# Kernel optimization log

Hardware: AMD Instinct MI355X
Metric: run time of the kernel (lower is better)

Reference implementation:

```python
import jax, jax.numpy as jnp
import numpy as np

N_NODES = 50000
N_EDGES = 800000
D = 64
N_GRAPHS = 512
N_LAYERS = 3
HID_FC = 64
N_CLASSES = 10


def setup_inputs() -> dict:
    key = jax.random.key(0)
    ks = jax.random.split(key, 12)
    s = 1.0 / np.sqrt(D)
    x = jax.random.normal(ks[0], (N_NODES, D), dtype=jnp.float32)
    edge_index = jax.random.randint(ks[1], (2, N_EDGES), 0, N_NODES, dtype=jnp.int32)
    batch = jnp.sort(jax.random.randint(ks[2], (N_NODES,), 0, N_GRAPHS, dtype=jnp.int32))
    convW1 = jax.random.normal(ks[3], (N_LAYERS, D, D), dtype=jnp.float32) * s
    convb1 = jax.random.normal(ks[4], (N_LAYERS, D), dtype=jnp.float32) * 0.01
    convW2 = jax.random.normal(ks[5], (N_LAYERS, D, D), dtype=jnp.float32) * s
    convb2 = jax.random.normal(ks[6], (N_LAYERS, D), dtype=jnp.float32) * 0.01
    fcW1 = jax.random.normal(ks[7], (D, HID_FC), dtype=jnp.float32) * s
    fcb1 = jax.random.normal(ks[8], (HID_FC,), dtype=jnp.float32) * 0.01
    fcW2 = jax.random.normal(ks[9], (HID_FC, N_CLASSES), dtype=jnp.float32) * (1.0 / np.sqrt(HID_FC))
    fcb2 = jax.random.normal(ks[10], (N_CLASSES,), dtype=jnp.float32) * 0.01
    return {"x": x, "convW1": convW1, "convb1": convb1, "convW2": convW2,
            "convb2": convb2, "fcW1": fcW1, "fcb1": fcb1, "fcW2": fcW2,
            "fcb2": fcb2, "edge_index": edge_index, "batch": batch}


def reference(x, convW1, convb1, convW2, convb2, fcW1, fcb1, fcW2, fcb2, edge_index, batch):
    src, dst = edge_index[0], edge_index[1]
    h = x
    for l in range(N_LAYERS):
        # GIN aggregation: (1 + eps) * x + sum_{j in N(i)} x_j, eps = 0
        agg = jax.ops.segment_sum(h[src], dst, num_segments=N_NODES)
        h = h + agg
        # per-layer MLP: Linear -> ReLU -> Linear
        h = jax.nn.relu(h @ convW1[l] + convb1[l])
        h = h @ convW2[l] + convb2[l]
    # global max pool over nodes of each graph
    g = jax.ops.segment_max(h, batch, num_segments=N_GRAPHS)
    # FC head: Linear(64) -> ReLU -> Linear(num_classes)
    g = jax.nn.relu(g @ fcW1 + fcb1)
    logits = g @ fcW2 + fcb2
    return jax.nn.log_softmax(logits, axis=1)
```

## Files before the change

### kernel.cpp

```cpp
#include <hip/hip_runtime.h>
#include <math.h>

#define N_NODES 50000
#define N_EDGES 800000
#define D 64
#define N_GRAPHS 512
#define N_CLASSES 10
#define NT 3125

#define SCAN_B 512
#define NB_SCAN ((N_NODES + SCAN_B - 1) / SCAN_B)

typedef __attribute__((ext_vector_type(8))) short bf16x8;
typedef __attribute__((ext_vector_type(4))) float f32x4;

#define MFMA16(a, b, c) __builtin_amdgcn_mfma_f32_16x16x32_bf16(a, b, c, 0, 0, 0)


__device__ __forceinline__ unsigned mapf(float f) {
  unsigned u = __float_as_uint(f);
  return (u & 0x80000000u) ? ~u : (u | 0x80000000u);
}
__device__ __forceinline__ float unmapf(unsigned u) {
  return __uint_as_float((u & 0x80000000u) ? (u & 0x7FFFFFFFu) : ~u);
}
__device__ __forceinline__ ushort bf16_rne(float f) {
  unsigned u = __float_as_uint(f);
  u += 0x7FFFu + ((u >> 16) & 1u);
  return (ushort)(u >> 16);
}
__device__ __forceinline__ float bf16_tof(ushort h) {
  return __uint_as_float(((unsigned)h) << 16);
}
__device__ __forceinline__ unsigned pack2(float a, float b) {
  return (unsigned)bf16_rne(a) | ((unsigned)bf16_rne(b) << 16);
}
__device__ __forceinline__ float2 unpack2(unsigned v) {
  return make_float2(__uint_as_float(v << 16), __uint_as_float(v & 0xFFFF0000u));
}


__global__ void to_bf16(const float* __restrict__ in, unsigned* __restrict__ out) {
  int i = blockIdx.x * 256 + threadIdx.x;
  float4 v = reinterpret_cast<const float4*>(in)[i];
  reinterpret_cast<uint2*>(out)[i] = make_uint2(pack2(v.x, v.y), pack2(v.z, v.w));
}


__global__ void wprep(const float* __restrict__ convW1, const float* __restrict__ convW2,
                      ushort* __restrict__ wf) {
  const int wi = blockIdx.x;
  const int layer = wi >> 1, which = wi & 1;
  const float* W = (which ? convW2 : convW1) + layer * 4096;
  const int t = threadIdx.x;
  const int f = t >> 6, lane = t & 63;
  const int ct = f >> 1, ks = f & 1;
  const int n = ct * 16 + (lane & 15);
  const int k0 = ks * 32 + ((lane >> 4) << 3);
  ushort hi[8], lo[8];
#pragma unroll
  for (int v = 0; v < 8; ++v) {
    float w = W[(k0 + v) * 64 + n];
    ushort h = bf16_rne(w);
    hi[v] = h;
    lo[v] = bf16_rne(w - bf16_tof(h));
  }
  ushort* base = wf + layer * 16384 + which * 8192;
  *(uint4*)(base + f * 512 + lane * 8) = *(uint4*)hi;
  *(uint4*)(base + 4096 + f * 512 + lane * 8) = *(uint4*)lo;
}


__global__ void hist_kernel(const int* __restrict__ dst, int* __restrict__ deg) {
  int e = blockIdx.x * 256 + threadIdx.x;
  if (e < N_EDGES) atomicAdd(&deg[dst[e]], 1);
}

__global__ void scan_blocks(const int* __restrict__ deg, int* __restrict__ bsum) {
  __shared__ int sd[SCAN_B];
  int i = blockIdx.x * SCAN_B + threadIdx.x;
  sd[threadIdx.x] = (i < N_NODES) ? deg[i] : 0;
  __syncthreads();
  for (int off = SCAN_B / 2; off > 0; off >>= 1) {
    if (threadIdx.x < off) sd[threadIdx.x] += sd[threadIdx.x + off];
    __syncthreads();
  }
  if (threadIdx.x == 0) bsum[blockIdx.x] = sd[0];
}

__global__ void scan_mid(int* __restrict__ bsum) {
  __shared__ int s[256];
  int t = threadIdx.x;
  if (t < NB_SCAN) s[t] = bsum[t];
  __syncthreads();
  if (t == 0) {
    int run = 0;
    for (int i = 0; i < NB_SCAN; ++i) { int v = s[i]; s[i] = run; run += v; }
  }
  __syncthreads();
  if (t < NB_SCAN) bsum[t] = s[t];
}

__global__ void scan_final(const int* __restrict__ deg, const int* __restrict__ bsum,
                           int* __restrict__ rs, int* __restrict__ cur) {
  __shared__ int sd[SCAN_B];
  int i = blockIdx.x * SCAN_B + threadIdx.x;
  int v = (i < N_NODES) ? deg[i] : 0;
  sd[threadIdx.x] = v;
  __syncthreads();
  for (int off = 1; off < SCAN_B; off <<= 1) {
    int add = (threadIdx.x >= off) ? sd[threadIdx.x - off] : 0;
    __syncthreads();
    sd[threadIdx.x] += add;
    __syncthreads();
  }
  if (i < N_NODES) {
    int ex = bsum[blockIdx.x] + sd[threadIdx.x] - v;
    rs[i] = ex;
    cur[i] = ex;
  }
  if (i == 0) rs[N_NODES] = N_EDGES;
}

__global__ void fill_csr(const int* __restrict__ src, const int* __restrict__ dst,
                         int* __restrict__ cur, int* __restrict__ csr) {
  int e = blockIdx.x * 256 + threadIdx.x;
  if (e >= N_EDGES) return;
  int p = atomicAdd(&cur[dst[e]], 1);
  csr[p] = src[e];
}


__global__ __launch_bounds__(256) void agg_bf16(
    const unsigned* __restrict__ hin, const int* __restrict__ csr,
    const int* __restrict__ rs, unsigned* __restrict__ hout) {
  const int t = threadIdx.x;
  const int hw = t >> 5, hl = t & 31;
  const int node = blockIdx.x * 8 + hw;
  float2 a = unpack2(hin[node * 32 + hl]);
  int e = rs[node];
  const int e1 = rs[node + 1];
  for (; e + 4 <= e1; e += 4) {
    int s0 = csr[e], s1 = csr[e + 1], s2 = csr[e + 2], s3 = csr[e + 3];
    float2 v0 = unpack2(hin[s0 * 32 + hl]);
    float2 v1 = unpack2(hin[s1 * 32 + hl]);
    float2 v2 = unpack2(hin[s2 * 32 + hl]);
    float2 v3 = unpack2(hin[s3 * 32 + hl]);
    a.x += v0.x + v1.x; a.y += v0.y + v1.y;
    a.x += v2.x + v3.x; a.y += v2.y + v3.y;
  }
  for (; e < e1; ++e) {
    float2 v = unpack2(hin[csr[e] * 32 + hl]);
    a.x += v.x; a.y += v.y;
  }
  hout[node * 32 + hl] = pack2(a.x, a.y);
}


template <int FINAL>
__global__ __launch_bounds__(256, 4) void mlp_bf16(
    unsigned* __restrict__ A,
    const ushort* __restrict__ wfL,
    const float* __restrict__ b1, const float* __restrict__ b2,
    const int* __restrict__ batch, unsigned* __restrict__ gU) {
  __shared__ ushort Wl[8192];
  __shared__ ushort tb[4][16 * 72];
  const int t = threadIdx.x;
  const int w = t >> 6, lane = t & 63;
  const int tile = blockIdx.x * 4 + w;
  const bool act = (tile < NT);
  const int m = lane & 15, g = lane >> 4;
  ushort* tw = tb[w];

  {
    const uint4* s = (const uint4*)wfL;
    uint4* d = (uint4*)Wl;
#pragma unroll
    for (int i = 0; i < 4; ++i) d[t + 256 * i] = s[t + 256 * i];
  }

  bf16x8 a0 = {}, a1 = {};
  if (act) {
    const ushort* Ar = (const ushort*)A + (size_t)(tile * 16 + m) * 64;
    a0 = *(const bf16x8*)(Ar + g * 8);
    a1 = *(const bf16x8*)(Ar + 32 + g * 8);
  }
  __syncthreads();

  const char* wb = (const char*)Wl + lane * 16;
#define LDW(off) (*(const bf16x8*)(wb + (off)))

  f32x4 c0 = {0.f, 0.f, 0.f, 0.f}, c1 = c0, c2 = c0, c3 = c0;
  bf16x8 h0 = {}, h1 = {};
  if (act) {
#define G1(ct, cc)                                     \
    cc = MFMA16(a0, LDW((2 * ct + 0) * 1024), cc);     \
    cc = MFMA16(a1, LDW((2 * ct + 1) * 1024), cc);     \
    cc = MFMA16(a0, LDW(8192 + (2 * ct + 0) * 1024), cc); \
    cc = MFMA16(a1, LDW(8192 + (2 * ct + 1) * 1024), cc);
    G1(0, c0) G1(1, c1) G1(2, c2) G1(3, c3)
#undef G1

    float bv0 = b1[m], bv1 = b1[16 + m], bv2 = b1[32 + m], bv3 = b1[48 + m];
#define WRT(cc, ct, bv)                                               \
    tw[(g * 4 + 0) * 72 + ct * 16 + m] = bf16_rne(fmaxf(cc[0] + bv, 0.f)); \
    tw[(g * 4 + 1) * 72 + ct * 16 + m] = bf16_rne(fmaxf(cc[1] + bv, 0.f)); \
    tw[(g * 4 + 2) * 72 + ct * 16 + m] = bf16_rne(fmaxf(cc[2] + bv, 0.f)); \
    tw[(g * 4 + 3) * 72 + ct * 16 + m] = bf16_rne(fmaxf(cc[3] + bv, 0.f));
    WRT(c0, 0, bv0) WRT(c1, 1, bv1) WRT(c2, 2, bv2) WRT(c3, 3, bv3)
#undef WRT
    h0 = *(const bf16x8*)(tw + m * 72 + g * 8);
    h1 = *(const bf16x8*)(tw + m * 72 + 32 + g * 8);
  }
  __syncthreads();

  {
    const uint4* s = (const uint4*)(wfL + 8192);
    uint4* d = (uint4*)Wl;
#pragma unroll
    for (int i = 0; i < 4; ++i) d[t + 256 * i] = s[t + 256 * i];
  }
  __syncthreads();

  if (act) {
    c0 = (f32x4){0.f, 0.f, 0.f, 0.f}; c1 = c0; c2 = c0; c3 = c0;
#define G2(ct, cc)                                     \
    cc = MFMA16(h0, LDW((2 * ct + 0) * 1024), cc);     \
    cc = MFMA16(h1, LDW((2 * ct + 1) * 1024), cc);     \
    cc = MFMA16(h0, LDW(8192 + (2 * ct + 0) * 1024), cc); \
    cc = MFMA16(h1, LDW(8192 + (2 * ct + 1) * 1024), cc);
    G2(0, c0) G2(1, c1) G2(2, c2) G2(3, c3)
#undef G2
#undef LDW

    float bv0 = b2[m], bv1 = b2[16 + m], bv2 = b2[32 + m], bv3 = b2[48 + m];
    if (FINAL) {
      int b40 = batch[tile * 16 + g * 4 + 0];
      int b41 = batch[tile * 16 + g * 4 + 1];
      int b42 = batch[tile * 16 + g * 4 + 2];
      int b43 = batch[tile * 16 + g * 4 + 3];
#define PM(cc, ct, bv)                                          \
      atomicMax(&gU[b40 * 64 + ct * 16 + m], mapf(cc[0] + bv)); \
      atomicMax(&gU[b41 * 64 + ct * 16 + m], mapf(cc[1] + bv)); \
      atomicMax(&gU[b42 * 64 + ct * 16 + m], mapf(cc[2] + bv)); \
      atomicMax(&gU[b43 * 64 + ct * 16 + m], mapf(cc[3] + bv));
      PM(c0, 0, bv0) PM(c1, 1, bv1) PM(c2, 2, bv2) PM(c3, 3, bv3)
#undef PM
    } else {
#define WRO(cc, ct, bv)                                    \
      tw[(g * 4 + 0) * 72 + ct * 16 + m] = bf16_rne(cc[0] + bv); \
      tw[(g * 4 + 1) * 72 + ct * 16 + m] = bf16_rne(cc[1] + bv); \
      tw[(g * 4 + 2) * 72 + ct * 16 + m] = bf16_rne(cc[2] + bv); \
      tw[(g * 4 + 3) * 72 + ct * 16 + m] = bf16_rne(cc[3] + bv);
      WRO(c0, 0, bv0) WRO(c1, 1, bv1) WRO(c2, 2, bv2) WRO(c3, 3, bv3)
#undef WRO
      uint4 v0 = *(const uint4*)(tw + m * 72 + g * 16);
      uint4 v1 = *(const uint4*)(tw + m * 72 + g * 16 + 8);
      uint4* Aw = (uint4*)((ushort*)A + (size_t)(tile * 16 + m) * 64 + g * 16);
      Aw[0] = v0;
      Aw[1] = v1;
    }
  }
}


__global__ void init_g(unsigned* __restrict__ gU) {
  int i = blockIdx.x * blockDim.x + threadIdx.x;
  if (i < N_GRAPHS * D) gU[i] = 0x007FFFFFu;
}

__global__ void head_kernel(const unsigned* __restrict__ gU,
                            const float* __restrict__ fcW1, const float* __restrict__ fcb1,
                            const float* __restrict__ fcW2, const float* __restrict__ fcb2,
                            float* __restrict__ out) {
  __shared__ float gbuf[64];
  __shared__ float hid[64];
  __shared__ float logit[N_CLASSES];
  __shared__ float red[2];
  const int gi = blockIdx.x;
  const int t = threadIdx.x;

  gbuf[t] = unmapf(gU[gi * D + t]);
  __syncthreads();

  float a = fcb1[t];
#pragma unroll
  for (int k = 0; k < 64; ++k) a = fmaf(gbuf[k], fcW1[k * 64 + t], a);
  hid[t] = fmaxf(a, 0.0f);
  __syncthreads();

  if (t < N_CLASSES) {
    float l = fcb2[t];
#pragma unroll
    for (int k = 0; k < 64; ++k) l = fmaf(hid[k], fcW2[k * N_CLASSES + t], l);
    logit[t] = l;
  }
  __syncthreads();

  if (t == 0) {
    float mx = logit[0];
    for (int i = 1; i < N_CLASSES; ++i) mx = fmaxf(mx, logit[i]);
    float s = 0.0f;
    for (int i = 0; i < N_CLASSES; ++i) s += expf(logit[i] - mx);
    red[0] = mx;
    red[1] = logf(s);
  }
  __syncthreads();

  if (t < N_CLASSES) out[gi * N_CLASSES + t] = logit[t] - red[0] - red[1];
}


extern "C" void kernel_launch(void* const* d_in, const int* in_sizes, int n_in,
                              void* d_out, int out_size, void* d_ws, size_t ws_size,
                              hipStream_t stream) {
  const float* x      = (const float*)d_in[0];
  const float* convW1 = (const float*)d_in[1];
  const float* convb1 = (const float*)d_in[2];
  const float* convW2 = (const float*)d_in[3];
  const float* convb2 = (const float*)d_in[4];
  const float* fcW1   = (const float*)d_in[5];
  const float* fcb1   = (const float*)d_in[6];
  const float* fcW2   = (const float*)d_in[7];
  const float* fcb2   = (const float*)d_in[8];
  const int*   edge   = (const int*)d_in[9];
  const int*   batch  = (const int*)d_in[10];
  float* out = (float*)d_out;

  const int* src = edge;
  const int* dst = edge + N_EDGES;

  unsigned* xb  = (unsigned*)d_ws;
  unsigned* hbA = xb + (size_t)N_NODES * 32;
  unsigned* gU  = hbA + (size_t)N_NODES * 32;
  int* rs  = (int*)(gU + N_GRAPHS * D);
  int* csr = rs + N_NODES + 1;
  ushort* wf = (ushort*)(csr + N_EDGES);
  int* deg  = (int*)hbA;
  int* cur  = deg + N_NODES;
  int* bsum = cur + N_NODES;

  to_bf16<<<(N_NODES * 16) / 256, 256, 0, stream>>>(x, xb);
  wprep<<<6, 512, 0, stream>>>(convW1, convW2, wf);
  init_g<<<(N_GRAPHS * D + 255) / 256, 256, 0, stream>>>(gU);

  hipMemsetAsync(deg, 0, N_NODES * sizeof(int), stream);
  hist_kernel<<<N_EDGES / 256, 256, 0, stream>>>(dst, deg);
  scan_blocks<<<NB_SCAN, SCAN_B, 0, stream>>>(deg, bsum);
  scan_mid<<<1, 256, 0, stream>>>(bsum);
  scan_final<<<NB_SCAN, SCAN_B, 0, stream>>>(deg, bsum, rs, cur);
  fill_csr<<<N_EDGES / 256, 256, 0, stream>>>(src, dst, cur, csr);

  const int AGG_B = N_NODES / 8;
  const int MLP_B = (NT + 3) / 4;
  agg_bf16<<<AGG_B, 256, 0, stream>>>(xb, csr, rs, hbA);
  mlp_bf16<0><<<MLP_B, 256, 0, stream>>>(hbA, wf, convb1, convb2, batch, gU);
  agg_bf16<<<AGG_B, 256, 0, stream>>>(hbA, csr, rs, xb);
  mlp_bf16<0><<<MLP_B, 256, 0, stream>>>(xb, wf + 16384, convb1 + 64, convb2 + 64,
                                         batch, gU);
  agg_bf16<<<AGG_B, 256, 0, stream>>>(xb, csr, rs, hbA);
  mlp_bf16<1><<<MLP_B, 256, 0, stream>>>(hbA, wf + 32768, convb1 + 128, convb2 + 128,
                                         batch, gU);

  head_kernel<<<N_GRAPHS, 64, 0, stream>>>(gU, fcW1, fcb1, fcW2, fcb2, out);
}
```

Measured before the change: 242.6 us.

## Partition CSR build by destination range and preload both MLP weights once

```diff
diff --git a/kernel.cpp b/kernel.cpp
--- a/kernel.cpp
+++ b/kernel.cpp
@@ -7,6 +7,7 @@
 #define N_GRAPHS 512
 #define N_CLASSES 10
 #define NT 3125
+#define NPART 6250
 
 #define SCAN_B 512
 #define NB_SCAN ((N_NODES + SCAN_B - 1) / SCAN_B)
@@ -71,9 +72,14 @@
 }
 
 
-__global__ void hist_kernel(const int* __restrict__ dst, int* __restrict__ deg) {
-  int e = blockIdx.x * 256 + threadIdx.x;
-  if (e < N_EDGES) atomicAdd(&deg[dst[e]], 1);
+__global__ void hist_part(const int* __restrict__ dst, int* __restrict__ deg) {
+  const int p = blockIdx.x & 7;
+  const int lo = p * NPART, hi = lo + NPART;
+  const int stride = (gridDim.x >> 3) * 256;
+  for (int e = (blockIdx.x >> 3) * 256 + threadIdx.x; e < N_EDGES; e += stride) {
+    int d = dst[e];
+    if (d >= lo && d < hi) atomicAdd(&deg[d], 1);
+  }
 }
 
 __global__ void scan_blocks(const int* __restrict__ deg, int* __restrict__ bsum) {
@@ -122,12 +128,18 @@
   if (i == 0) rs[N_NODES] = N_EDGES;
 }
 
-__global__ void fill_csr(const int* __restrict__ src, const int* __restrict__ dst,
-                         int* __restrict__ cur, int* __restrict__ csr) {
-  int e = blockIdx.x * 256 + threadIdx.x;
-  if (e >= N_EDGES) return;
-  int p = atomicAdd(&cur[dst[e]], 1);
-  csr[p] = src[e];
+__global__ void fill_part(const int* __restrict__ src, const int* __restrict__ dst,
+                          int* __restrict__ cur, int* __restrict__ csr) {
+  const int p = blockIdx.x & 7;
+  const int lo = p * NPART, hi = lo + NPART;
+  const int stride = (gridDim.x >> 3) * 256;
+  for (int e = (blockIdx.x >> 3) * 256 + threadIdx.x; e < N_EDGES; e += stride) {
+    int d = dst[e];
+    if (d >= lo && d < hi) {
+      int pos = atomicAdd(&cur[d], 1);
+      csr[pos] = src[e];
+    }
+  }
 }
 
 
@@ -158,12 +170,13 @@
 
 
 template <int FINAL>
-__global__ __launch_bounds__(256, 4) void mlp_bf16(
-    unsigned* __restrict__ A,
+__global__ __launch_bounds__(256, 2) void mlp_bf16(
+    const unsigned* __restrict__ Ain,
+    unsigned* __restrict__ Aout,
     const ushort* __restrict__ wfL,
     const float* __restrict__ b1, const float* __restrict__ b2,
     const int* __restrict__ batch, unsigned* __restrict__ gU) {
-  __shared__ ushort Wl[8192];
+  __shared__ ushort Wl[16384];
   __shared__ ushort tb[4][16 * 72];
   const int t = threadIdx.x;
   const int w = t >> 6, lane = t & 63;
@@ -176,12 +189,12 @@
     const uint4* s = (const uint4*)wfL;
     uint4* d = (uint4*)Wl;
 #pragma unroll
-    for (int i = 0; i < 4; ++i) d[t + 256 * i] = s[t + 256 * i];
+    for (int i = 0; i < 8; ++i) d[t + 256 * i] = s[t + 256 * i];
   }
 
   bf16x8 a0 = {}, a1 = {};
   if (act) {
-    const ushort* Ar = (const ushort*)A + (size_t)(tile * 16 + m) * 64;
+    const ushort* Ar = (const ushort*)Ain + (size_t)(tile * 16 + m) * 64;
     a0 = *(const bf16x8*)(Ar + g * 8);
     a1 = *(const bf16x8*)(Ar + 32 + g * 8);
   }
@@ -190,50 +203,38 @@
   const char* wb = (const char*)Wl + lane * 16;
 #define LDW(off) (*(const bf16x8*)(wb + (off)))
 
-  f32x4 c0 = {0.f, 0.f, 0.f, 0.f}, c1 = c0, c2 = c0, c3 = c0;
-  bf16x8 h0 = {}, h1 = {};
   if (act) {
-#define G1(ct, cc)                                     \
-    cc = MFMA16(a0, LDW((2 * ct + 0) * 1024), cc);     \
-    cc = MFMA16(a1, LDW((2 * ct + 1) * 1024), cc);     \
+    f32x4 c0 = {0.f, 0.f, 0.f, 0.f}, c1 = c0, c2 = c0, c3 = c0;
+#define G1(ct, cc)                                        \
+    cc = MFMA16(a0, LDW((2 * ct + 0) * 1024), cc);        \
+    cc = MFMA16(a1, LDW((2 * ct + 1) * 1024), cc);        \
     cc = MFMA16(a0, LDW(8192 + (2 * ct + 0) * 1024), cc); \
     cc = MFMA16(a1, LDW(8192 + (2 * ct + 1) * 1024), cc);
     G1(0, c0) G1(1, c1) G1(2, c2) G1(3, c3)
 #undef G1
 
     float bv0 = b1[m], bv1 = b1[16 + m], bv2 = b1[32 + m], bv3 = b1[48 + m];
-#define WRT(cc, ct, bv)                                               \
-    tw[(g * 4 + 0) * 72 + ct * 16 + m] = bf16_rne(fmaxf(cc[0] + bv, 0.f)); \
-    tw[(g * 4 + 1) * 72 + ct * 16 + m] = bf16_rne(fmaxf(cc[1] + bv, 0.f)); \
-    tw[(g * 4 + 2) * 72 + ct * 16 + m] = bf16_rne(fmaxf(cc[2] + bv, 0.f)); \
+#define WRT(cc, ct, bv)                                                     \
+    tw[(g * 4 + 0) * 72 + ct * 16 + m] = bf16_rne(fmaxf(cc[0] + bv, 0.f));  \
+    tw[(g * 4 + 1) * 72 + ct * 16 + m] = bf16_rne(fmaxf(cc[1] + bv, 0.f));  \
+    tw[(g * 4 + 2) * 72 + ct * 16 + m] = bf16_rne(fmaxf(cc[2] + bv, 0.f));  \
     tw[(g * 4 + 3) * 72 + ct * 16 + m] = bf16_rne(fmaxf(cc[3] + bv, 0.f));
     WRT(c0, 0, bv0) WRT(c1, 1, bv1) WRT(c2, 2, bv2) WRT(c3, 3, bv3)
 #undef WRT
-    h0 = *(const bf16x8*)(tw + m * 72 + g * 8);
-    h1 = *(const bf16x8*)(tw + m * 72 + 32 + g * 8);
-  }
-  __syncthreads();
-
-  {
-    const uint4* s = (const uint4*)(wfL + 8192);
-    uint4* d = (uint4*)Wl;
-#pragma unroll
-    for (int i = 0; i < 4; ++i) d[t + 256 * i] = s[t + 256 * i];
-  }
-  __syncthreads();
-
-  if (act) {
+    bf16x8 h0 = *(const bf16x8*)(tw + m * 72 + g * 8);
+    bf16x8 h1 = *(const bf16x8*)(tw + m * 72 + 32 + g * 8);
+
     c0 = (f32x4){0.f, 0.f, 0.f, 0.f}; c1 = c0; c2 = c0; c3 = c0;
-#define G2(ct, cc)                                     \
-    cc = MFMA16(h0, LDW((2 * ct + 0) * 1024), cc);     \
-    cc = MFMA16(h1, LDW((2 * ct + 1) * 1024), cc);     \
-    cc = MFMA16(h0, LDW(8192 + (2 * ct + 0) * 1024), cc); \
-    cc = MFMA16(h1, LDW(8192 + (2 * ct + 1) * 1024), cc);
+#define G2(ct, cc)                                         \
+    cc = MFMA16(h0, LDW(16384 + (2 * ct + 0) * 1024), cc); \
+    cc = MFMA16(h1, LDW(16384 + (2 * ct + 1) * 1024), cc); \
+    cc = MFMA16(h0, LDW(24576 + (2 * ct + 0) * 1024), cc); \
+    cc = MFMA16(h1, LDW(24576 + (2 * ct + 1) * 1024), cc);
     G2(0, c0) G2(1, c1) G2(2, c2) G2(3, c3)
 #undef G2
 #undef LDW
 
-    float bv0 = b2[m], bv1 = b2[16 + m], bv2 = b2[32 + m], bv3 = b2[48 + m];
+    float bv20 = b2[m], bv21 = b2[16 + m], bv22 = b2[32 + m], bv23 = b2[48 + m];
     if (FINAL) {
       int b40 = batch[tile * 16 + g * 4 + 0];
       int b41 = batch[tile * 16 + g * 4 + 1];
@@ -244,21 +245,22 @@
       atomicMax(&gU[b41 * 64 + ct * 16 + m], mapf(cc[1] + bv)); \
       atomicMax(&gU[b42 * 64 + ct * 16 + m], mapf(cc[2] + bv)); \
       atomicMax(&gU[b43 * 64 + ct * 16 + m], mapf(cc[3] + bv));
-      PM(c0, 0, bv0) PM(c1, 1, bv1) PM(c2, 2, bv2) PM(c3, 3, bv3)
+      PM(c0, 0, bv20) PM(c1, 1, bv21) PM(c2, 2, bv22) PM(c3, 3, bv23)
 #undef PM
     } else {
-#define WRO(cc, ct, bv)                                    \
+#define WRO(cc, ct, bv)                                          \
       tw[(g * 4 + 0) * 72 + ct * 16 + m] = bf16_rne(cc[0] + bv); \
       tw[(g * 4 + 1) * 72 + ct * 16 + m] = bf16_rne(cc[1] + bv); \
       tw[(g * 4 + 2) * 72 + ct * 16 + m] = bf16_rne(cc[2] + bv); \
       tw[(g * 4 + 3) * 72 + ct * 16 + m] = bf16_rne(cc[3] + bv);
-      WRO(c0, 0, bv0) WRO(c1, 1, bv1) WRO(c2, 2, bv2) WRO(c3, 3, bv3)
+      WRO(c0, 0, bv20) WRO(c1, 1, bv21) WRO(c2, 2, bv22) WRO(c3, 3, bv23)
 #undef WRO
-      uint4 v0 = *(const uint4*)(tw + m * 72 + g * 16);
-      uint4 v1 = *(const uint4*)(tw + m * 72 + g * 16 + 8);
-      uint4* Aw = (uint4*)((ushort*)A + (size_t)(tile * 16 + m) * 64 + g * 16);
-      Aw[0] = v0;
-      Aw[1] = v1;
+      const int r = lane >> 2, q = lane & 3;
+      uint4 v0 = *(const uint4*)(tw + r * 72 + q * 16);
+      uint4 v1 = *(const uint4*)(tw + r * 72 + q * 16 + 8);
+      ushort* Ao = (ushort*)Aout + (size_t)tile * 1024;
+      *(uint4*)(Ao + lane * 16) = v0;
+      *(uint4*)(Ao + lane * 16 + 8) = v1;
     }
   }
 }
@@ -332,11 +334,12 @@
 
   unsigned* xb  = (unsigned*)d_ws;
   unsigned* hbA = xb + (size_t)N_NODES * 32;
-  unsigned* gU  = hbA + (size_t)N_NODES * 32;
+  unsigned* hbB = hbA + (size_t)N_NODES * 32;
+  unsigned* gU  = hbB + (size_t)N_NODES * 32;
   int* rs  = (int*)(gU + N_GRAPHS * D);
   int* csr = rs + N_NODES + 1;
   ushort* wf = (ushort*)(csr + N_EDGES);
-  int* deg  = (int*)hbA;
+  int* deg  = (int*)hbB;
   int* cur  = deg + N_NODES;
   int* bsum = cur + N_NODES;
 
@@ -345,22 +348,22 @@
   init_g<<<(N_GRAPHS * D + 255) / 256, 256, 0, stream>>>(gU);
 
   hipMemsetAsync(deg, 0, N_NODES * sizeof(int), stream);
-  hist_kernel<<<N_EDGES / 256, 256, 0, stream>>>(dst, deg);
+  hist_part<<<2048, 256, 0, stream>>>(dst, deg);
   scan_blocks<<<NB_SCAN, SCAN_B, 0, stream>>>(deg, bsum);
   scan_mid<<<1, 256, 0, stream>>>(bsum);
   scan_final<<<NB_SCAN, SCAN_B, 0, stream>>>(deg, bsum, rs, cur);
-  fill_csr<<<N_EDGES / 256, 256, 0, stream>>>(src, dst, cur, csr);
+  fill_part<<<2048, 256, 0, stream>>>(src, dst, cur, csr);
 
   const int AGG_B = N_NODES / 8;
   const int MLP_B = (NT + 3) / 4;
   agg_bf16<<<AGG_B, 256, 0, stream>>>(xb, csr, rs, hbA);
-  mlp_bf16<0><<<MLP_B, 256, 0, stream>>>(hbA, wf, convb1, convb2, batch, gU);
-  agg_bf16<<<AGG_B, 256, 0, stream>>>(hbA, csr, rs, xb);
-  mlp_bf16<0><<<MLP_B, 256, 0, stream>>>(xb, wf + 16384, convb1 + 64, convb2 + 64,
+  mlp_bf16<0><<<MLP_B, 256, 0, stream>>>(hbA, hbB, wf, convb1, convb2, batch, gU);
+  agg_bf16<<<AGG_B, 256, 0, stream>>>(hbB, csr, rs, hbA);
+  mlp_bf16<0><<<MLP_B, 256, 0, stream>>>(hbA, xb, wf + 16384, convb1 + 64, convb2 + 64,
                                          batch, gU);
   agg_bf16<<<AGG_B, 256, 0, stream>>>(xb, csr, rs, hbA);
-  mlp_bf16<1><<<MLP_B, 256, 0, stream>>>(hbA, wf + 32768, convb1 + 128, convb2 + 128,
-                                         batch, gU);
+  mlp_bf16<1><<<MLP_B, 256, 0, stream>>>(hbA, nullptr, wf + 32768, convb1 + 128,
+                                         convb2 + 128, batch, gU);
 
   head_kernel<<<N_GRAPHS, 64, 0, stream>>>(gU, fcW1, fcb1, fcW2, fcb2, out);
 }
```

Result: faster. 228.7 us (-5.7%).
